# Performance work log

Measured on AMD Instinct MI355X. Metric: run time of the kernel, lower is better.

The kernel has to match this reference:

```python
import jax, jax.numpy as jnp
import numpy as np

BATCH, SEQ_LEN, VEC_DIM, WIDTH = 64, 256, 512, 3


def setup_inputs() -> dict:
    key = jax.random.key(0)
    k = jax.random.split(key, 8)
    F0r = jax.random.normal(k[0], (BATCH, SEQ_LEN, VEC_DIM), jnp.float32)
    F1r = jax.random.normal(k[1], (BATCH, SEQ_LEN, VEC_DIM), jnp.float32)
    sent0_mask = (jax.random.uniform(k[2], (BATCH, SEQ_LEN)) < 0.9).astype(jnp.float32)
    sent1_mask = (jax.random.uniform(k[3], (BATCH, SEQ_LEN)) < 0.9).astype(jnp.float32)
    # nn.Parameter(torch.randn(seq_len, vec_dim))
    W0 = jax.random.normal(k[4], (SEQ_LEN, VEC_DIM), jnp.float32)
    W1 = jax.random.normal(k[5], (SEQ_LEN, VEC_DIM), jnp.float32)
    # Conv2d(2, 1, kernel_size=(WIDTH, 1)) default init: U(-1/sqrt(fan_in), +)
    bound = 1.0 / np.sqrt(2 * WIDTH * 1)
    conv_w = jax.random.uniform(k[6], (1, 2, WIDTH, 1), jnp.float32, -bound, bound)
    conv_b = jax.random.uniform(k[7], (1,), jnp.float32, -bound, bound)
    return dict(F0r=F0r, F1r=F1r, sent0_mask=sent0_mask, sent1_mask=sent1_mask,
                W0=W0, W1=W1, conv_w=conv_w, conv_b=conv_b)


def _conv_tanh_pool(x, conv_w, conv_b):
    # x: [B, 2, S, D]; conv pad (WIDTH-1, 0) -> [B, 1, S+WIDTH-1, D]
    y = jax.lax.conv_general_dilated(
        x, conv_w, window_strides=(1, 1),
        padding=((WIDTH - 1, WIDTH - 1), (0, 0)),
        dimension_numbers=('NCHW', 'OIHW', 'NCHW'))
    y = jnp.tanh(y + conv_b[None, :, None, None])
    # AvgPool2d kernel (WIDTH,1), stride 1 -> [B, 1, S, D]
    y = jax.lax.reduce_window(y, 0.0, jax.lax.add,
                              (1, 1, WIDTH, 1), (1, 1, 1, 1), 'VALID') / WIDTH
    return y[:, 0]  # squeeze channel -> [B, S, D]


def reference(F0r, F1r, sent0_mask, sent1_mask, W0, W1, conv_w, conv_b):
    # masking is in-place in the torch code, so masked F0/F1 feed the conv too
    F0 = F0r * sent0_mask[:, :, None]  # [B, S, D]
    F1 = F1r * sent1_mask[:, :, None]
    # pairwise L2 via ||u-v||^2 = ||u||^2 + ||v||^2 - 2 u.v (avoids [B,S,S,D])
    sq0 = jnp.sum(F0 * F0, axis=-1)  # [B, S]
    sq1 = jnp.sum(F1 * F1, axis=-1)
    cross = jnp.einsum('bid,bjd->bij', F0, F1)  # [B, S, S]
    d2 = jnp.maximum(sq0[:, :, None] + sq1[:, None, :] - 2.0 * cross, 0.0)
    norm = jnp.where(d2 > 0, jnp.sqrt(jnp.where(d2 > 0, d2, 1.0)), 0.0)
    A = 1.0 / (1.0 + norm)  # [B, S, S]
    F0a = jnp.einsum('bij,id->bjd', A, W0)  # A^T @ W0
    F1a = jnp.einsum('bij,jd->bid', A, W1)  # A @ W1
    x0 = jnp.stack([F0, F0a], axis=1)  # [B, 2, S, D]
    x1 = jnp.stack([F1, F1a], axis=1)
    out0 = _conv_tanh_pool(x0, conv_w, conv_b)
    out1 = _conv_tanh_pool(x1, conv_w, conv_b)
    return out0, out1
```

## Files before the change

### kernel.cpp

```cpp
#include <hip/hip_runtime.h>

typedef unsigned short u16;
typedef __attribute__((ext_vector_type(8))) short short8;
typedef __attribute__((ext_vector_type(4))) float f32x4;

__device__ inline u16 f2bf(float f) {
    union { float f; unsigned u; } v; v.f = f;
    unsigned u = v.u;
    unsigned r = (u + 0x7FFFu + ((u >> 16) & 1u)) >> 16;
    return (u16)r;
}
__device__ inline float bf2f(u16 h) {
    union { unsigned u; float f; } v; v.u = ((unsigned)h) << 16;
    return v.f;
}
__device__ inline float frcp(float x) { return __builtin_amdgcn_rcpf(x); }
__device__ inline float fsqrt(float x) { return __builtin_amdgcn_sqrtf(x); }
__device__ inline float ftanh(float x) {
    float e = __expf(2.f * x);
    return 1.f - 2.f * frcp(e + 1.f);
}
__device__ inline float4 bf4f(ushort4 u) {
    float4 f; f.x = bf2f(u.x); f.y = bf2f(u.y); f.z = bf2f(u.z); f.w = bf2f(u.w);
    return f;
}

typedef const __attribute__((address_space(1))) void* gas_ptr;
typedef __attribute__((address_space(3))) void* las_ptr;
__device__ __forceinline__ void gl2lds16(const u16* g, u16* l) {
    __builtin_amdgcn_global_load_lds((gas_ptr)(const void*)g, (las_ptr)(void*)l, 16, 0, 0);
}

__global__ __launch_bounds__(128) void prep_kernel(
    const float* __restrict__ F0r, const float* __restrict__ F1r,
    const float* __restrict__ m0, const float* __restrict__ m1,
    const float* __restrict__ W0, const float* __restrict__ W1,
    u16* __restrict__ F0b, u16* __restrict__ F1b,
    u16* __restrict__ WT0, u16* __restrict__ WT1,
    float* __restrict__ sq0, float* __restrict__ sq1)
{
    int bx = blockIdx.x;
    int t = threadIdx.x;
    if (bx >= 16384) {
        __shared__ u16 Wl[64][40];
        int idx2 = bx - 16384;
        int a = idx2 >> 6;
        int tile = idx2 & 63;
        int s0 = (tile >> 3) * 32, d0 = (tile & 7) * 64;
        const float* W = a ? W1 : W0;
        u16* WT = a ? WT1 : WT0;
        #pragma unroll
        for (int i = 0; i < 4; ++i) {
            int idx = i * 512 + t * 4;
            int sl = idx >> 6, dl = idx & 63;
            float4 v = *(const float4*)(W + (size_t)(s0 + sl) * 512 + d0 + dl);
            Wl[dl + 0][sl] = f2bf(v.x);
            Wl[dl + 1][sl] = f2bf(v.y);
            Wl[dl + 2][sl] = f2bf(v.z);
            Wl[dl + 3][sl] = f2bf(v.w);
        }
        __syncthreads();
        #pragma unroll
        for (int i = 0; i < 4; ++i) {
            int idx = i * 512 + t * 4;
            int dl = idx >> 5, sl = idx & 31;
            ushort4 v;
            v.x = Wl[dl][sl + 0]; v.y = Wl[dl][sl + 1];
            v.z = Wl[dl][sl + 2]; v.w = Wl[dl][sl + 3];
            *(ushort4*)(WT + (size_t)(d0 + dl) * 256 + s0 + sl) = v;
        }
        return;
    }
    int bs = bx;
    size_t base = (size_t)bs * 512 + t * 4;
    float mk0 = m0[bs], mk1 = m1[bs];
    float4 v0 = *(const float4*)(F0r + base);
    float4 v1 = *(const float4*)(F1r + base);
    v0.x *= mk0; v0.y *= mk0; v0.z *= mk0; v0.w *= mk0;
    v1.x *= mk1; v1.y *= mk1; v1.z *= mk1; v1.w *= mk1;
    ushort4 u0; u0.x = f2bf(v0.x); u0.y = f2bf(v0.y); u0.z = f2bf(v0.z); u0.w = f2bf(v0.w);
    ushort4 u1; u1.x = f2bf(v1.x); u1.y = f2bf(v1.y); u1.z = f2bf(v1.z); u1.w = f2bf(v1.w);
    *(ushort4*)(F0b + base) = u0;
    *(ushort4*)(F1b + base) = u1;
    float s0p = v0.x*v0.x + v0.y*v0.y + v0.z*v0.z + v0.w*v0.w;
    float s1p = v1.x*v1.x + v1.y*v1.y + v1.z*v1.z + v1.w*v1.w;
    #pragma unroll
    for (int off = 32; off > 0; off >>= 1) {
        s0p += __shfl_xor(s0p, off);
        s1p += __shfl_xor(s1p, off);
    }
    __shared__ float red0[2], red1[2];
    if ((t & 63) == 0) { red0[t >> 6] = s0p; red1[t >> 6] = s1p; }
    __syncthreads();
    if (t == 0) { sq0[bs] = red0[0] + red0[1]; sq1[bs] = red1[0] + red1[1]; }
}

__global__ __launch_bounds__(256) void fused_kernel(
    const u16* __restrict__ F0b, const u16* __restrict__ F1b,
    const float* __restrict__ sq0, const float* __restrict__ sq1,
    const u16* __restrict__ WT0, const u16* __restrict__ WT1,
    const u16* __restrict__ F0b2, const u16* __restrict__ F1b2,
    const float* __restrict__ cw, const float* __restrict__ cb,
    float* __restrict__ out)
{
    __shared__ __align__(16) u16 Al[36][264];
    __shared__ __align__(16) u16 region[21136];
    u16 (*Fl)[132] = (u16(*)[132])(region + 16384);

    int b = blockIdx.y, side = blockIdx.z;
    int s0 = blockIdx.x * 32;
    const u16* Sp  = (side ? F0b : F1b) + (size_t)b * 131072;
    const u16* Gp  = (side ? F1b : F0b) + (size_t)b * 131072;
    const float* sqS = (side ? sq0 : sq1) + b * 256;
    const float* sqG = (side ? sq1 : sq0) + b * 256;
    const u16* WT = side ? WT1 : WT0;
    const u16* Fb = (side ? F1b : F0b) + (size_t)b * 131072;
    float* o = out + (size_t)side * 8388608 + (size_t)b * 131072;

    const int t = threadIdx.x;
    const int lane = t & 63, w = t >> 6;
    const int q = lane >> 4, lm = lane & 15;

    f32x4 acc1[3][4];
    #pragma unroll
    for (int x = 0; x < 3; ++x)
        #pragma unroll
        for (int cn = 0; cn < 4; ++cn)
            acc1[x][cn] = (f32x4){0.f, 0.f, 0.f, 0.f};

    for (int kc = 0; kc < 512; kc += 64) {
        __syncthreads();
        #pragma unroll
        for (int i = 0; i < 8; ++i) {
            int idx = i * 256 + t;
            int r = idx >> 3, seg = idx & 7;
            int ss = seg ^ (r & 7);
            gl2lds16(Gp + (size_t)r * 512 + kc + ss * 8,
                     &region[(i * 256 + w * 64) * 8]);
        }
        {
            int idx = t;
            int r = idx >> 3, seg = idx & 7;
            int ss = seg ^ (r & 7);
            int s = s0 - 2 + r; s = s < 0 ? 0 : (s > 255 ? 255 : s);
            gl2lds16(Sp + (size_t)s * 512 + kc + ss * 8,
                     &region[16384 + (w * 64) * 8]);
        }
        if (t < 128) {
            int idx = 256 + t;
            int r = idx >> 3, seg = idx & 7;
            int ss = seg ^ (r & 7);
            int s = s0 - 2 + r; s = s < 0 ? 0 : (s > 255 ? 255 : s);
            gl2lds16(Sp + (size_t)s * 512 + kc + ss * 8,
                     &region[16384 + (256 + w * 64) * 8]);
        }
        __syncthreads();
        #pragma unroll
        for (int ks = 0; ks < 64; ks += 32) {
            int su = (((ks >> 3) + q) ^ (lm & 7)) * 8;
            short8 af[3], bfr[4];
            #pragma unroll
            for (int x = 0; x < 3; ++x)
                af[x] = *(const short8*)&region[16384 + (x * 16 + lm) * 64 + su];
            #pragma unroll
            for (int cn = 0; cn < 4; ++cn)
                bfr[cn] = *(const short8*)&region[(w * 64 + cn * 16 + lm) * 64 + su];
            #pragma unroll
            for (int x = 0; x < 3; ++x)
                #pragma unroll
                for (int cn = 0; cn < 4; ++cn)
                    acc1[x][cn] = __builtin_amdgcn_mfma_f32_16x16x32_bf16(
                        af[x], bfr[cn], acc1[x][cn], 0, 0, 0);
        }
    }
    __syncthreads();

    float sqg[4];
    #pragma unroll
    for (int cn = 0; cn < 4; ++cn) sqg[cn] = sqG[w * 64 + cn * 16 + lm];
    #pragma unroll
    for (int x = 0; x < 3; ++x) {
        #pragma unroll
        for (int r = 0; r < 4; ++r) {
            int m = x * 16 + q * 4 + r;
            if (m < 36) {
                int s = s0 - 2 + m;
                bool ok = (unsigned)s < 256u;
                float sqs = ok ? sqS[s] : 0.f;
                #pragma unroll
                for (int cn = 0; cn < 4; ++cn) {
                    float d2 = fmaxf(sqs + sqg[cn] - 2.f * acc1[x][cn][r], 0.f);
                    float a = ok ? frcp(1.f + fsqrt(d2)) : 0.f;
                    Al[m][w * 64 + cn * 16 + lm] = f2bf(a);
                }
            }
        }
    }

#define STAGE_B(bufo, nn, kb) do {                                             \
    _Pragma("unroll")                                                          \
    for (int i_ = 0; i_ < 4; ++i_) {                                           \
        int idx_ = i_ * 256 + t;                                               \
        int r_ = idx_ >> 3, seg_ = idx_ & 7;                                   \
        int ss_ = seg_ ^ (r_ & 7);                                             \
        gl2lds16(WT + (size_t)((nn) + r_) * 256 + (kb) + ss_ * 8,              \
                 &region[(bufo) + (i_ * 256 + w * 64) * 8]);                   \
    } } while (0)

    const u16* aRow[3];
    aRow[0] = &Al[lm][0];
    aRow[1] = &Al[16 + lm][0];
    aRow[2] = &Al[(lm < 4) ? (32 + lm) : 0][0];

    float w00 = cw[0], w01 = cw[1], w02 = cw[2];
    float w10 = cw[3], w11 = cw[4], w12 = cw[5];
    float bias = cb[0];
    const float third = 1.f / 3.f;
    const int g = t >> 5;
    const int dl = (t & 31) * 4;

    STAGE_B(0, 0, 0);

    for (int n0 = 0; n0 < 512; n0 += 128) {
        f32x4 acc[3][2];
        #pragma unroll
        for (int x = 0; x < 3; ++x)
            #pragma unroll
            for (int y = 0; y < 2; ++y)
                acc[x][y] = (f32x4){0.f, 0.f, 0.f, 0.f};

        #pragma unroll
        for (int kb_i = 0; kb_i < 4; ++kb_i) {
            __syncthreads();
            if (kb_i < 3)
                STAGE_B(((kb_i + 1) & 1) * 8192, n0, (kb_i + 1) * 64);
            const int cbuf = (kb_i & 1) * 8192;
            const int kb = kb_i * 64;
            #pragma unroll
            for (int ks = 0; ks < 64; ks += 32) {
                short8 af[3], bfr[2];
                #pragma unroll
                for (int x = 0; x < 3; ++x)
                    af[x] = *(const short8*)(aRow[x] + kb + ks + q * 8);
                #pragma unroll
                for (int y = 0; y < 2; ++y) {
                    int rb = w * 32 + y * 16 + lm;
                    int su = (((ks >> 3) + q) ^ (lm & 7)) * 8;
                    bfr[y] = *(const short8*)&region[cbuf + rb * 64 + su];
                }
                #pragma unroll
                for (int x = 0; x < 3; ++x)
                    #pragma unroll
                    for (int y = 0; y < 2; ++y)
                        acc[x][y] = __builtin_amdgcn_mfma_f32_16x16x32_bf16(
                            af[x], bfr[y], acc[x][y], 0, 0, 0);
            }
        }

        ushort4 frg[8];
        #pragma unroll
        for (int k = 0; k < 8; ++k) {
            int s = s0 + g * 4 - 2 + k;
            ushort4 z = {0, 0, 0, 0};
            frg[k] = ((unsigned)s < 256u)
                   ? *(const ushort4*)(Fb + (size_t)s * 512 + n0 + dl) : z;
        }

        #pragma unroll
        for (int x = 0; x < 3; ++x)
            #pragma unroll
            for (int r = 0; r < 4; ++r) {
                int m = x * 16 + q * 4 + r;
                if (m < 36) {
                    #pragma unroll
                    for (int y = 0; y < 2; ++y)
                        Fl[m][w * 32 + y * 16 + lm] = f2bf(acc[x][y][r]);
                }
            }
        __syncthreads();

        if (n0 < 384)
            STAGE_B(0, n0 + 128, 0);

        float4 f[8], a[8];
        #pragma unroll
        for (int k = 0; k < 8; ++k) {
            f[k] = bf4f(frg[k]);
            a[k] = bf4f(*(const ushort4*)&Fl[g * 4 + k][dl]);
        }
        float4 ty[6];
        #pragma unroll
        for (int k = 0; k < 6; ++k) {
            float4 y;
            y.x = bias + w00*f[k].x + w01*f[k+1].x + w02*f[k+2].x + w10*a[k].x + w11*a[k+1].x + w12*a[k+2].x;
            y.y = bias + w00*f[k].y + w01*f[k+1].y + w02*f[k+2].y + w10*a[k].y + w11*a[k+1].y + w12*a[k+2].y;
            y.z = bias + w00*f[k].z + w01*f[k+1].z + w02*f[k+2].z + w10*a[k].z + w11*a[k+1].z + w12*a[k+2].z;
            y.w = bias + w00*f[k].w + w01*f[k+1].w + w02*f[k+2].w + w10*a[k].w + w11*a[k+1].w + w12*a[k+2].w;
            y.x = ftanh(y.x); y.y = ftanh(y.y); y.z = ftanh(y.z); y.w = ftanh(y.w);
            ty[k] = y;
        }
        #pragma unroll
        for (int r = 0; r < 4; ++r) {
            float4 res;
            res.x = (ty[r].x + ty[r+1].x + ty[r+2].x) * third;
            res.y = (ty[r].y + ty[r+1].y + ty[r+2].y) * third;
            res.z = (ty[r].z + ty[r+1].z + ty[r+2].z) * third;
            res.w = (ty[r].w + ty[r+1].w + ty[r+2].w) * third;
            *(float4*)(o + (size_t)(s0 + g * 4 + r) * 512 + n0 + dl) = res;
        }
    }
#undef STAGE_B
}

extern "C" void kernel_launch(void* const* d_in, const int* in_sizes, int n_in,
                              void* d_out, int out_size, void* d_ws, size_t ws_size,
                              hipStream_t stream)
{
    const float* F0r = (const float*)d_in[0];
    const float* F1r = (const float*)d_in[1];
    const float* m0  = (const float*)d_in[2];
    const float* m1  = (const float*)d_in[3];
    const float* W0  = (const float*)d_in[4];
    const float* W1  = (const float*)d_in[5];
    const float* cw  = (const float*)d_in[6];
    const float* cb  = (const float*)d_in[7];
    float* out = (float*)d_out;

    char* ws = (char*)d_ws;
    u16* F0b   = (u16*)(ws);
    u16* F1b   = (u16*)(ws + 16777216);
    float* sq0 = (float*)(ws + 50331648);
    float* sq1 = (float*)(ws + 50397184);
    u16* WT0   = (u16*)(ws + 50462720);
    u16* WT1   = (u16*)(ws + 50724864);

    prep_kernel<<<16512, 128, 0, stream>>>(F0r, F1r, m0, m1, W0, W1,
                                           F0b, F1b, WT0, WT1, sq0, sq1);
    fused_kernel<<<dim3(8, 64, 2), 256, 0, stream>>>(F0b, F1b, sq0, sq1,
                                                     WT0, WT1, F0b, F1b,
                                                     cw, cb, out);
}
```

Baseline: 208.1 us.

## Make prep kernel grid-stride per-wave rows and remap fused block order

The prep kernel changes from one 128-thread block per row (16384 blocks) to 1024 blocks of 256 threads. Each wave handles whole rows in a grid-stride loop, loading 8 floats per lane, and the LDS reduction and barrier are gone. The W transpose blocks now use 256 threads with half the loop trips. The fused kernel remaps its linear block index so that consecutive blocks cover different batches and sides before different row tiles, which changes L2 locality across concurrently scheduled blocks.

```diff
diff --git a/kernel.cpp b/kernel.cpp
--- a/kernel.cpp
+++ b/kernel.cpp
@@ -31,7 +31,7 @@
     __builtin_amdgcn_global_load_lds((gas_ptr)(const void*)g, (las_ptr)(void*)l, 16, 0, 0);
 }
 
-__global__ __launch_bounds__(128) void prep_kernel(
+__global__ __launch_bounds__(256) void prep_kernel(
     const float* __restrict__ F0r, const float* __restrict__ F1r,
     const float* __restrict__ m0, const float* __restrict__ m1,
     const float* __restrict__ W0, const float* __restrict__ W1,
@@ -41,19 +41,19 @@
 {
     int bx = blockIdx.x;
     int t = threadIdx.x;
-    if (bx >= 16384) {
+    if (bx >= 1024) {
         __shared__ u16 Wl[64][40];
-        int idx2 = bx - 16384;
+        int idx2 = bx - 1024;
         int a = idx2 >> 6;
         int tile = idx2 & 63;
-        int s0 = (tile >> 3) * 32, d0 = (tile & 7) * 64;
+        int s0t = (tile >> 3) * 32, d0 = (tile & 7) * 64;
         const float* W = a ? W1 : W0;
         u16* WT = a ? WT1 : WT0;
         #pragma unroll
-        for (int i = 0; i < 4; ++i) {
-            int idx = i * 512 + t * 4;
+        for (int i = 0; i < 2; ++i) {
+            int idx = i * 1024 + t * 4;
             int sl = idx >> 6, dl = idx & 63;
-            float4 v = *(const float4*)(W + (size_t)(s0 + sl) * 512 + d0 + dl);
+            float4 v = *(const float4*)(W + (size_t)(s0t + sl) * 512 + d0 + dl);
             Wl[dl + 0][sl] = f2bf(v.x);
             Wl[dl + 1][sl] = f2bf(v.y);
             Wl[dl + 2][sl] = f2bf(v.z);
@@ -61,45 +61,55 @@
         }
         __syncthreads();
         #pragma unroll
-        for (int i = 0; i < 4; ++i) {
-            int idx = i * 512 + t * 4;
+        for (int i = 0; i < 2; ++i) {
+            int idx = i * 1024 + t * 4;
             int dl = idx >> 5, sl = idx & 31;
             ushort4 v;
             v.x = Wl[dl][sl + 0]; v.y = Wl[dl][sl + 1];
             v.z = Wl[dl][sl + 2]; v.w = Wl[dl][sl + 3];
-            *(ushort4*)(WT + (size_t)(d0 + dl) * 256 + s0 + sl) = v;
+            *(ushort4*)(WT + (size_t)(d0 + dl) * 256 + s0t + sl) = v;
         }
         return;
     }
-    int bs = bx;
-    size_t base = (size_t)bs * 512 + t * 4;
-    float mk0 = m0[bs], mk1 = m1[bs];
-    float4 v0 = *(const float4*)(F0r + base);
-    float4 v1 = *(const float4*)(F1r + base);
-    v0.x *= mk0; v0.y *= mk0; v0.z *= mk0; v0.w *= mk0;
-    v1.x *= mk1; v1.y *= mk1; v1.z *= mk1; v1.w *= mk1;
-    ushort4 u0; u0.x = f2bf(v0.x); u0.y = f2bf(v0.y); u0.z = f2bf(v0.z); u0.w = f2bf(v0.w);
-    ushort4 u1; u1.x = f2bf(v1.x); u1.y = f2bf(v1.y); u1.z = f2bf(v1.z); u1.w = f2bf(v1.w);
-    *(ushort4*)(F0b + base) = u0;
-    *(ushort4*)(F1b + base) = u1;
-    float s0p = v0.x*v0.x + v0.y*v0.y + v0.z*v0.z + v0.w*v0.w;
-    float s1p = v1.x*v1.x + v1.y*v1.y + v1.z*v1.z + v1.w*v1.w;
-    #pragma unroll
-    for (int off = 32; off > 0; off >>= 1) {
-        s0p += __shfl_xor(s0p, off);
-        s1p += __shfl_xor(s1p, off);
-    }
-    __shared__ float red0[2], red1[2];
-    if ((t & 63) == 0) { red0[t >> 6] = s0p; red1[t >> 6] = s1p; }
-    __syncthreads();
-    if (t == 0) { sq0[bs] = red0[0] + red0[1]; sq1[bs] = red1[0] + red1[1]; }
+    int gw = (bx << 2) + (t >> 6);
+    int lane = t & 63;
+    for (int row = gw; row < 16384; row += 4096) {
+        size_t base = (size_t)row * 512 + lane * 8;
+        float mk0 = m0[row], mk1 = m1[row];
+        float4 a0 = *(const float4*)(F0r + base);
+        float4 a1 = *(const float4*)(F0r + base + 4);
+        float4 b0 = *(const float4*)(F1r + base);
+        float4 b1 = *(const float4*)(F1r + base + 4);
+        a0.x *= mk0; a0.y *= mk0; a0.z *= mk0; a0.w *= mk0;
+        a1.x *= mk0; a1.y *= mk0; a1.z *= mk0; a1.w *= mk0;
+        b0.x *= mk1; b0.y *= mk1; b0.z *= mk1; b0.w *= mk1;
+        b1.x *= mk1; b1.y *= mk1; b1.z *= mk1; b1.w *= mk1;
+        ushort4 u0a, u0b, u1a, u1b;
+        u0a.x = f2bf(a0.x); u0a.y = f2bf(a0.y); u0a.z = f2bf(a0.z); u0a.w = f2bf(a0.w);
+        u0b.x = f2bf(a1.x); u0b.y = f2bf(a1.y); u0b.z = f2bf(a1.z); u0b.w = f2bf(a1.w);
+        u1a.x = f2bf(b0.x); u1a.y = f2bf(b0.y); u1a.z = f2bf(b0.z); u1a.w = f2bf(b0.w);
+        u1b.x = f2bf(b1.x); u1b.y = f2bf(b1.y); u1b.z = f2bf(b1.z); u1b.w = f2bf(b1.w);
+        *(ushort4*)(F0b + base)     = u0a;
+        *(ushort4*)(F0b + base + 4) = u0b;
+        *(ushort4*)(F1b + base)     = u1a;
+        *(ushort4*)(F1b + base + 4) = u1b;
+        float s0p = a0.x*a0.x + a0.y*a0.y + a0.z*a0.z + a0.w*a0.w
+                  + a1.x*a1.x + a1.y*a1.y + a1.z*a1.z + a1.w*a1.w;
+        float s1p = b0.x*b0.x + b0.y*b0.y + b0.z*b0.z + b0.w*b0.w
+                  + b1.x*b1.x + b1.y*b1.y + b1.z*b1.z + b1.w*b1.w;
+        #pragma unroll
+        for (int off = 32; off > 0; off >>= 1) {
+            s0p += __shfl_xor(s0p, off);
+            s1p += __shfl_xor(s1p, off);
+        }
+        if (lane == 0) { sq0[row] = s0p; sq1[row] = s1p; }
+    }
 }
 
 __global__ __launch_bounds__(256) void fused_kernel(
     const u16* __restrict__ F0b, const u16* __restrict__ F1b,
     const float* __restrict__ sq0, const float* __restrict__ sq1,
     const u16* __restrict__ WT0, const u16* __restrict__ WT1,
-    const u16* __restrict__ F0b2, const u16* __restrict__ F1b2,
     const float* __restrict__ cw, const float* __restrict__ cb,
     float* __restrict__ out)
 {
@@ -107,8 +117,13 @@
     __shared__ __align__(16) u16 region[21136];
     u16 (*Fl)[132] = (u16(*)[132])(region + 16384);
 
-    int b = blockIdx.y, side = blockIdx.z;
-    int s0 = blockIdx.x * 32;
+    int L = blockIdx.x + (blockIdx.y << 3) + (blockIdx.z << 9);
+    int qq = L >> 6, rr = L & 63;
+    int s0i = rr >> 3;
+    int code = qq * 8 + (rr & 7);
+    int b = code >> 1, side = code & 1;
+    int s0 = s0i * 32;
+
     const u16* Sp  = (side ? F0b : F1b) + (size_t)b * 131072;
     const u16* Gp  = (side ? F1b : F0b) + (size_t)b * 131072;
     const float* sqS = (side ? sq0 : sq1) + b * 256;
@@ -334,9 +349,8 @@
     u16* WT0   = (u16*)(ws + 50462720);
     u16* WT1   = (u16*)(ws + 50724864);
 
-    prep_kernel<<<16512, 128, 0, stream>>>(F0r, F1r, m0, m1, W0, W1,
-                                           F0b, F1b, WT0, WT1, sq0, sq1);
+    prep_kernel<<<1152, 256, 0, stream>>>(F0r, F1r, m0, m1, W0, W1,
+                                          F0b, F1b, WT0, WT1, sq0, sq1);
     fused_kernel<<<dim3(8, 64, 2), 256, 0, stream>>>(F0b, F1b, sq0, sq1,
-                                                     WT0, WT1, F0b, F1b,
-                                                     cw, cb, out);
-}
+                                                     WT0, WT1, cw, cb, out);
+}
```

Result: faster. 188.9 us (-9.2%).
